# Performance work log

Hardware: AMD Instinct MI355X
Metric: run time of the kernel (lower is better)

Reference implementation:

```python
import jax, jax.numpy as jnp
import numpy as np

N, E, H = 100000, 3200000, 128


def setup_inputs() -> dict:
    key = jax.random.key(0)
    ks = jax.random.split(key, 12)
    s = 1.0 / np.sqrt(H)
    x = jax.random.normal(ks[0], (N, H), dtype=jnp.float32)
    edge_index = jax.random.randint(ks[1], (2, E), 0, N, dtype=jnp.int64)
    # GatedGraphConv weight: [num_layers=1, H, H] -> single [H, H]
    W = jax.random.normal(ks[2], (H, H), dtype=jnp.float32) * s
    # GRUCell (gate order: r, z, n)
    gru_w_ih = jax.random.normal(ks[3], (3 * H, H), dtype=jnp.float32) * s
    gru_w_hh = jax.random.normal(ks[4], (3 * H, H), dtype=jnp.float32) * s
    gru_b_ih = jax.random.normal(ks[5], (3 * H,), dtype=jnp.float32) * s
    gru_b_hh = jax.random.normal(ks[6], (3 * H,), dtype=jnp.float32) * s
    # LSTM layer 0 (gate order: i, f, g, o)
    lstm_w_ih = jax.random.normal(ks[7], (4 * H, H), dtype=jnp.float32) * s
    lstm_w_hh = jax.random.normal(ks[8], (4 * H, H), dtype=jnp.float32) * s
    lstm_b_ih = jax.random.normal(ks[9], (4 * H,), dtype=jnp.float32) * s
    lstm_b_hh = jax.random.normal(ks[10], (4 * H,), dtype=jnp.float32) * s
    return {
        "x": x, "edge_index": edge_index, "W": W,
        "gru_w_ih": gru_w_ih, "gru_w_hh": gru_w_hh,
        "gru_b_ih": gru_b_ih, "gru_b_hh": gru_b_hh,
        "lstm_w_ih": lstm_w_ih, "lstm_w_hh": lstm_w_hh,
        "lstm_b_ih": lstm_b_ih, "lstm_b_hh": lstm_b_hh,
    }


def _forward(x, edge_index, W, gru_w_ih, gru_w_hh, gru_b_ih, gru_b_hh,
             lstm_w_ih, lstm_w_hh, lstm_b_ih, lstm_b_hh):
    n = x.shape[0]
    src, dst = edge_index[0], edge_index[1]
    # GatedGraphConv, num_layers=1, mean aggregation
    m = x @ W                                   # [N, H]
    msg = m[src]                                # [E, H] gather (memory-bound)
    agg_sum = jax.ops.segment_sum(msg, dst, num_segments=n)
    deg = jax.ops.segment_sum(jnp.ones((src.shape[0],), x.dtype), dst, num_segments=n)
    agg = agg_sum / jnp.maximum(deg, 1.0)[:, None]
    # GRUCell(agg, x): gates r, z, n
    gi = agg @ gru_w_ih.T + gru_b_ih
    gh = x @ gru_w_hh.T + gru_b_hh
    i_r, i_z, i_n = jnp.split(gi, 3, axis=-1)
    h_r, h_z, h_n = jnp.split(gh, 3, axis=-1)
    r = jax.nn.sigmoid(i_r + h_r)
    z = jax.nn.sigmoid(i_z + h_z)
    ng = jnp.tanh(i_n + r * h_n)
    h_conv = (1.0 - z) * ng + z * x             # conv output H_tilde
    # 1-layer LSTM over seq_len=1 with zero initial (H, C)
    gates = h_conv @ lstm_w_ih.T + lstm_b_ih + lstm_b_hh  # h0 = 0
    i_g, f_g, g_g, o_g = jnp.split(gates, 4, axis=-1)
    c = jax.nn.sigmoid(i_g) * jnp.tanh(g_g)
    h_lstm = jax.nn.sigmoid(o_g) * jnp.tanh(c)
    return jax.nn.relu(h_lstm)


def reference(x, edge_index, W, gru_w_ih, gru_w_hh, gru_b_ih, gru_b_hh,
              lstm_w_ih, lstm_w_hh, lstm_b_ih, lstm_b_hh):
    return _forward(x, edge_index, W, gru_w_ih, gru_w_hh, gru_b_ih, gru_b_hh,
                    lstm_w_ih, lstm_w_hh, lstm_b_ih, lstm_b_hh)
```

## Files before the change

kernel.cpp:

```cpp
#include <hip/hip_runtime.h>
#include <math.h>

#define HD 128
#define PB 512
#define SCB 4096

typedef __attribute__((ext_vector_type(8))) short short8;
typedef __attribute__((ext_vector_type(4))) float f32x4;
typedef __attribute__((ext_vector_type(2))) float f32x2;
typedef __attribute__((ext_vector_type(4))) unsigned u32x4;

__device__ __forceinline__ float sigf(float v) { return 1.0f / (1.0f + __expf(-v)); }
__device__ __forceinline__ float tanhf_fast(float v) {
  float e = __expf(2.0f * v);
  return 1.0f - 2.0f / (e + 1.0f);
}

__device__ __forceinline__ unsigned short f2bf(float f) {
  union { float f; unsigned u; } v; v.f = f;
  unsigned r = (v.u + 0x7fffu + ((v.u >> 16) & 1u)) >> 16;
  return (unsigned short)r;
}
__device__ __forceinline__ float bf2f(unsigned short b) {
  union { unsigned u; float f; } v; v.u = ((unsigned)b) << 16;
  return v.f;
}


__global__ __launch_bounds__(256) void bcount_k(const int* __restrict__ ei,
                                                int* __restrict__ bcnt,
                                                int E, int N, int shift, int NB) {
  __shared__ int h[256];
  const int blk = blockIdx.x, tid = threadIdx.x;
  h[tid] = 0;
  __syncthreads();
  int per = (E + PB - 1) / PB;
  int lo = blk * per;
  int hi = (lo + per < E) ? lo + per : E;
  for (int e = lo + tid; e < hi; e += 256) {
    int d = ei[(size_t)E + e];
    if ((unsigned)d >= (unsigned)N) continue;
    atomicAdd(&h[d >> shift], 1);
  }
  __syncthreads();
  if (tid < NB) bcnt[tid * PB + blk] = h[tid];
}

__global__ __launch_bounds__(256) void scan1_k(const int* __restrict__ a,
                                               int* __restrict__ bsums, int total) {
  __shared__ int ts[256];
  int b = blockIdx.x, tid = threadIdx.x;
  int lo = b * SCB + tid * 16;
  int s = 0;
#pragma unroll
  for (int i = 0; i < 16; ++i) {
    int idx = lo + i;
    if (idx < total) s += a[idx];
  }
  ts[tid] = s;
  __syncthreads();
  for (int off = 128; off > 0; off >>= 1) {
    if (tid < off) ts[tid] += ts[tid + off];
    __syncthreads();
  }
  if (tid == 0) bsums[b] = ts[0];
}

__global__ __launch_bounds__(256) void scan2_k(int* __restrict__ bsums, int nb) {
  __shared__ int ts[256];
  int tid = threadIdx.x;
  int v = (tid < nb) ? bsums[tid] : 0;
  ts[tid] = v;
  __syncthreads();
  for (int off = 1; off < 256; off <<= 1) {
    int u = (tid >= off) ? ts[tid - off] : 0;
    __syncthreads();
    ts[tid] += u;
    __syncthreads();
  }
  if (tid < nb) bsums[tid] = ts[tid] - v;
}

__global__ __launch_bounds__(256) void scan3_k(int* __restrict__ a,
                                               const int* __restrict__ bsums,
                                               int total, int nblk) {
  __shared__ int ts[256];
  int b = blockIdx.x, tid = threadIdx.x;
  int lo = b * SCB + tid * 16;
  int pre[16];
  int s = 0;
#pragma unroll
  for (int i = 0; i < 16; ++i) {
    int idx = lo + i;
    int xv = (idx < total) ? a[idx] : 0;
    pre[i] = s;
    s += xv;
  }
  ts[tid] = s;
  __syncthreads();
  for (int off = 1; off < 256; off <<= 1) {
    int u = (tid >= off) ? ts[tid - off] : 0;
    __syncthreads();
    ts[tid] += u;
    __syncthreads();
  }
  int off0 = ts[tid] - s + bsums[b];
#pragma unroll
  for (int i = 0; i < 16; ++i) {
    int idx = lo + i;
    if (idx < total) a[idx] = off0 + pre[i];
  }
  if (b == nblk - 1 && tid == 255) a[total] = off0 + s;
}

__global__ __launch_bounds__(256) void bpart_k(const int* __restrict__ ei,
                                               const int* __restrict__ bstart,
                                               unsigned* __restrict__ ebuf,
                                               int E, int N, int shift, int NB,
                                               int sbits) {
  __shared__ int cur[256];
  const int blk = blockIdx.x, tid = threadIdx.x;
  if (tid < NB) cur[tid] = bstart[tid * PB + blk];
  __syncthreads();
  int per = (E + PB - 1) / PB;
  int lo = blk * per;
  int hi = (lo + per < E) ? lo + per : E;
  const unsigned dmask = (1u << shift) - 1u;
  for (int e = lo + tid; e < hi; e += 256) {
    int s = ei[e];
    int d = ei[(size_t)E + e];
    if ((unsigned)s >= (unsigned)N || (unsigned)d >= (unsigned)N) continue;
    int p = atomicAdd(&cur[d >> shift], 1);
    ebuf[p] = (((unsigned)d & dmask) << sbits) | (unsigned)s;
  }
}

__global__ __launch_bounds__(256) void bfill2_k(const unsigned* __restrict__ ebuf,
                                                const int* __restrict__ bstart,
                                                int* __restrict__ rowstart,
                                                int* __restrict__ csr,
                                                int N, int shift, int NB, int sbits) {
  __shared__ int cnt[2048];
  __shared__ int tsum[256];
  const int b = blockIdx.x, tid = threadIdx.x;
  const int d0 = b << shift;
  int dmax = d0 + (1 << shift);
  if (dmax > N) dmax = N;
  const int nd = dmax - d0;
  const unsigned smask = (1u << sbits) - 1u;
  for (int i = tid; i < nd; i += 256) cnt[i] = 0;
  __syncthreads();
  const int base = bstart[b * PB];
  const int end = bstart[(b + 1) * PB];
  for (int idx = base + tid; idx < end; idx += 256)
    atomicAdd(&cnt[ebuf[idx] >> sbits], 1);
  __syncthreads();
  const int C = (nd + 255) / 256;
  int lo = tid * C;
  int hi = (lo + C < nd) ? lo + C : nd;
  int loc[8];
  int s = 0;
  for (int i = lo; i < hi; ++i) {
    loc[i - lo] = cnt[i];
    s += cnt[i];
  }
  tsum[tid] = s;
  __syncthreads();
  for (int off = 1; off < 256; off <<= 1) {
    int u = (tid >= off) ? tsum[tid - off] : 0;
    __syncthreads();
    tsum[tid] += u;
    __syncthreads();
  }
  int run = tsum[tid] - s + base;
  for (int i = lo; i < hi; ++i) {
    rowstart[d0 + i] = run;
    cnt[i] = run;
    run += loc[i - lo];
  }
  if (b == NB - 1 && tid == 255) rowstart[N] = end;
  __syncthreads();
  for (int idx = base + tid; idx < end; idx += 256) {
    unsigned pk = ebuf[idx];
    int p = atomicAdd(&cnt[pk >> sbits], 1);
    csr[p] = (int)(pk & smask);
  }
}


__global__ __launch_bounds__(256) void convx_k(const float* __restrict__ x,
                                               unsigned short* __restrict__ xb,
                                               unsigned* __restrict__ x8, int n4) {
  int t = blockIdx.x * 256 + threadIdx.x;
  if (t >= n4) return;
  float4 v = reinterpret_cast<const float4*>(x)[t];
  ushort4 o;
  o.x = f2bf(v.x); o.y = f2bf(v.y); o.z = f2bf(v.z); o.w = f2bf(v.w);
  reinterpret_cast<ushort4*>(xb)[t] = o;
  int p8 = 0;
  p8 = __builtin_amdgcn_cvt_pk_fp8_f32(v.x, v.y, p8, false);
  p8 = __builtin_amdgcn_cvt_pk_fp8_f32(v.z, v.w, p8, true);
  x8[t] = (unsigned)p8;
}

__global__ __launch_bounds__(256) void prepw_k(
    const float* __restrict__ gwhh, const float* __restrict__ lwih,
    const float* __restrict__ lbih, const float* __restrict__ lbhh,
    unsigned short* __restrict__ gwhhb, unsigned short* __restrict__ lwb,
    float* __restrict__ lbias) {
  int t = blockIdx.x * 256 + threadIdx.x;
  if (t < 49152) { gwhhb[t] = f2bf(gwhh[t]); return; }
  t -= 49152;
  if (t < 49152) {
    int j = t >> 7, k = t & 127;
    int jm = j < 128 ? j : j + 128;
    lwb[t] = f2bf(lwih[(size_t)jm * 128 + k]);
    return;
  }
  t -= 49152;
  if (t < 384) {
    int jm = t < 128 ? t : t + 128;
    lbias[t] = lbih[jm] + lbhh[jm];
  }
}

__global__ __launch_bounds__(256) void prepbp_k(const float* __restrict__ W,
                                                const float* __restrict__ gwih,
                                                unsigned short* __restrict__ Bpb) {
  int t = blockIdx.x * 256 + threadIdx.x;
  if (t >= 49152) return;
  int j = t >> 7, k = t & 127;
  const float4* wr = reinterpret_cast<const float4*>(W + (size_t)k * 128);
  const float4* gr = reinterpret_cast<const float4*>(gwih + (size_t)j * 128);
  float acc = 0.f;
#pragma unroll
  for (int c = 0; c < 32; ++c) {
    float4 a = wr[c], b = gr[c];
    acc += a.x * b.x + a.y * b.y + a.z * b.z + a.w * b.w;
  }
  Bpb[t] = f2bf(acc);
}

__device__ __forceinline__ void accf8(f32x2* acc, uint4 v) {
  acc[0] += __builtin_amdgcn_cvt_pk_f32_fp8((int)v.x, false);
  acc[1] += __builtin_amdgcn_cvt_pk_f32_fp8((int)v.x, true);
  acc[2] += __builtin_amdgcn_cvt_pk_f32_fp8((int)v.y, false);
  acc[3] += __builtin_amdgcn_cvt_pk_f32_fp8((int)v.y, true);
  acc[4] += __builtin_amdgcn_cvt_pk_f32_fp8((int)v.z, false);
  acc[5] += __builtin_amdgcn_cvt_pk_f32_fp8((int)v.z, true);
  acc[6] += __builtin_amdgcn_cvt_pk_f32_fp8((int)v.w, false);
  acc[7] += __builtin_amdgcn_cvt_pk_f32_fp8((int)v.w, true);
}

__global__ __launch_bounds__(256) void gather_f8_k(const int* __restrict__ csr,
                                                   const int* __restrict__ rowstart,
                                                   const unsigned* __restrict__ x8,
                                                   unsigned short* __restrict__ xaggb,
                                                   int row0, int rowend) {
  int w = row0 + (int)(((long long)blockIdx.x * 256 + threadIdx.x) >> 6);
  if (w >= rowend) return;
  const int lane = threadIdx.x & 63;
  const int sub = lane >> 3, li = lane & 7;
  const int beg = rowstart[w], end = rowstart[w + 1];
  const uint4* x4 = reinterpret_cast<const uint4*>(x8);

  f32x2 acc[8];
#pragma unroll
  for (int i = 0; i < 8; ++i) acc[i] = (f32x2)0.f;

  int j = beg;
  for (; j + 16 <= end; j += 16) {
    int s0 = __builtin_nontemporal_load(&csr[j + sub]);
    int s1 = __builtin_nontemporal_load(&csr[j + 8 + sub]);
    uint4 v0 = x4[(size_t)s0 * 8 + li];
    uint4 v1 = x4[(size_t)s1 * 8 + li];
    accf8(acc, v0);
    accf8(acc, v1);
  }
  for (; j + 8 <= end; j += 8) {
    int s0 = __builtin_nontemporal_load(&csr[j + sub]);
    uint4 v0 = x4[(size_t)s0 * 8 + li];
    accf8(acc, v0);
  }
  int rem = end - j;
  if (sub < rem) {
    int s0 = csr[j + sub];
    uint4 v0 = x4[(size_t)s0 * 8 + li];
    accf8(acc, v0);
  }

  float a16[16];
#pragma unroll
  for (int i = 0; i < 8; ++i) { a16[2 * i] = acc[i].x; a16[2 * i + 1] = acc[i].y; }
#pragma unroll
  for (int i = 0; i < 16; ++i) {
    a16[i] += __shfl_xor(a16[i], 8, 64);
    a16[i] += __shfl_xor(a16[i], 16, 64);
    a16[i] += __shfl_xor(a16[i], 32, 64);
  }

  if (lane < 8) {
    float scale = 1.0f / fmaxf((float)(end - beg), 1.0f);
    u32x4 o1, o2;
    o1.x = (unsigned)f2bf(a16[0] * scale) | ((unsigned)f2bf(a16[1] * scale) << 16);
    o1.y = (unsigned)f2bf(a16[2] * scale) | ((unsigned)f2bf(a16[3] * scale) << 16);
    o1.z = (unsigned)f2bf(a16[4] * scale) | ((unsigned)f2bf(a16[5] * scale) << 16);
    o1.w = (unsigned)f2bf(a16[6] * scale) | ((unsigned)f2bf(a16[7] * scale) << 16);
    o2.x = (unsigned)f2bf(a16[8] * scale) | ((unsigned)f2bf(a16[9] * scale) << 16);
    o2.y = (unsigned)f2bf(a16[10] * scale) | ((unsigned)f2bf(a16[11] * scale) << 16);
    o2.z = (unsigned)f2bf(a16[12] * scale) | ((unsigned)f2bf(a16[13] * scale) << 16);
    o2.w = (unsigned)f2bf(a16[14] * scale) | ((unsigned)f2bf(a16[15] * scale) << 16);
    u32x4* dst = reinterpret_cast<u32x4*>(xaggb + (size_t)w * HD) + li * 2;
    dst[0] = o1;
    dst[1] = o2;
  }
}

__global__ __launch_bounds__(256) void gru_fused_k(
    const unsigned short* __restrict__ xaggb, const unsigned short* __restrict__ xb,
    const unsigned short* __restrict__ Bpb, const unsigned short* __restrict__ gwhhb,
    const float* __restrict__ gbih, const float* __restrict__ gbhh,
    unsigned short* __restrict__ hconv, int nrows, int nt) {
  __shared__ unsigned short Bsm[3][32][136];
  const int id = blockIdx.x;
  const int rest = id >> 3;
  const int cg = rest & 3;
  const int t = ((rest >> 2) << 3) | (id & 7);
  if (t >= nt) return;
  const int tid = threadIdx.x;
  const int w = tid >> 6, lane = tid & 63;
  const int q = lane >> 4, r = lane & 15;
  const int row0 = t * 64;
  const int c0 = cg * 32;

  int arow = row0 + (w << 4) + r;
  int ar = arow < nrows ? arow : nrows - 1;
  const unsigned short* Aa = xaggb + (size_t)ar * HD + q * 8;
  const unsigned short* Ax = xb + (size_t)ar * HD + q * 8;
  short8 a1[4], a2[4];
#pragma unroll
  for (int ks = 0; ks < 4; ++ks) {
    a1[ks] = *reinterpret_cast<const short8*>(Aa + ks * 32);
    a2[ks] = *reinterpret_cast<const short8*>(Ax + ks * 32);
  }

  f32x4 acc[6][2];
#pragma unroll
  for (int p = 0; p < 6; ++p)
#pragma unroll
    for (int cb = 0; cb < 2; ++cb) acc[p][cb] = (f32x4)0.f;

#pragma unroll
  for (int it = 0; it < 6; ++it) {
    int idx = it * 256 + tid;
    int p = idx >> 9, rem = idx & 511;
    int col = rem >> 4, kq = rem & 15;
    uint4 v = *reinterpret_cast<const uint4*>(
        Bpb + ((size_t)(p * 128 + c0 + col)) * HD + kq * 8);
    *reinterpret_cast<uint4*>(&Bsm[p][col][kq * 8]) = v;
  }
  __syncthreads();
#pragma unroll
  for (int ks = 0; ks < 4; ++ks)
#pragma unroll
    for (int p = 0; p < 3; ++p)
#pragma unroll
      for (int cb = 0; cb < 2; ++cb) {
        short8 bf = *reinterpret_cast<const short8*>(&Bsm[p][cb * 16 + r][ks * 32 + q * 8]);
        acc[p][cb] = __builtin_amdgcn_mfma_f32_16x16x32_bf16(a1[ks], bf, acc[p][cb], 0, 0, 0);
      }
  __syncthreads();

#pragma unroll
  for (int it = 0; it < 6; ++it) {
    int idx = it * 256 + tid;
    int p = idx >> 9, rem = idx & 511;
    int col = rem >> 4, kq = rem & 15;
    uint4 v = *reinterpret_cast<const uint4*>(
        gwhhb + ((size_t)(p * 128 + c0 + col)) * HD + kq * 8);
    *reinterpret_cast<uint4*>(&Bsm[p][col][kq * 8]) = v;
  }
  __syncthreads();
#pragma unroll
  for (int ks = 0; ks < 4; ++ks)
#pragma unroll
    for (int p = 0; p < 3; ++p)
#pragma unroll
      for (int cb = 0; cb < 2; ++cb) {
        short8 bf = *reinterpret_cast<const short8*>(&Bsm[p][cb * 16 + r][ks * 32 + q * 8]);
        acc[3 + p][cb] = __builtin_amdgcn_mfma_f32_16x16x32_bf16(a2[ks], bf, acc[3 + p][cb], 0, 0, 0);
      }

#pragma unroll
  for (int cb = 0; cb < 2; ++cb) {
    int col = c0 + cb * 16 + r;
    float bir = gbih[col], biz = gbih[col + 128], bin = gbih[col + 256];
    float bhr = gbhh[col], bhz = gbhh[col + 128], bhn = gbhh[col + 256];
#pragma unroll
    for (int reg = 0; reg < 4; ++reg) {
      int row = row0 + (w << 4) + q * 4 + reg;
      if (row < nrows) {
        float ir = acc[0][cb][reg] + bir, iz = acc[1][cb][reg] + biz;
        float inn = acc[2][cb][reg] + bin;
        float hr = acc[3][cb][reg] + bhr, hz = acc[4][cb][reg] + bhz;
        float hn = acc[5][cb][reg] + bhn;
        float rr = sigf(ir + hr), zz = sigf(iz + hz);
        float nn = tanhf_fast(inn + rr * hn);
        float xv = bf2f(xb[(size_t)row * HD + col]);
        hconv[(size_t)row * HD + col] = f2bf((1.f - zz) * nn + zz * xv);
      }
    }
  }
}

__global__ __launch_bounds__(256) void lstm_fused_k(
    const unsigned short* __restrict__ hconv, const unsigned short* __restrict__ lwb,
    const float* __restrict__ lbias, float* __restrict__ out, int nrows, int nt) {
  __shared__ unsigned short Bsm[3][32][136];
  const int id = blockIdx.x;
  const int rest = id >> 3;
  const int cg = rest & 3;
  const int t = ((rest >> 2) << 3) | (id & 7);
  if (t >= nt) return;
  const int tid = threadIdx.x;
  const int w = tid >> 6, lane = tid & 63;
  const int q = lane >> 4, r = lane & 15;
  const int row0 = t * 64;
  const int c0 = cg * 32;

  int arow = row0 + (w << 4) + r;
  int ar = arow < nrows ? arow : nrows - 1;
  const unsigned short* Ap = hconv + (size_t)ar * HD + q * 8;
  short8 hp[4];
#pragma unroll
  for (int ks = 0; ks < 4; ++ks)
    hp[ks] = *reinterpret_cast<const short8*>(Ap + ks * 32);

#pragma unroll
  for (int it = 0; it < 6; ++it) {
    int idx = it * 256 + tid;
    int p = idx >> 9, rem = idx & 511;
    int col = rem >> 4, kq = rem & 15;
    uint4 v = *reinterpret_cast<const uint4*>(
        lwb + ((size_t)(p * 128 + c0 + col)) * HD + kq * 8);
    *reinterpret_cast<uint4*>(&Bsm[p][col][kq * 8]) = v;
  }
  __syncthreads();

  f32x4 acc[3][2];
#pragma unroll
  for (int p = 0; p < 3; ++p)
#pragma unroll
    for (int cb = 0; cb < 2; ++cb) acc[p][cb] = (f32x4)0.f;

#pragma unroll
  for (int ks = 0; ks < 4; ++ks)
#pragma unroll
    for (int p = 0; p < 3; ++p)
#pragma unroll
      for (int cb = 0; cb < 2; ++cb) {
        short8 bf = *reinterpret_cast<const short8*>(&Bsm[p][cb * 16 + r][ks * 32 + q * 8]);
        acc[p][cb] = __builtin_amdgcn_mfma_f32_16x16x32_bf16(hp[ks], bf, acc[p][cb], 0, 0, 0);
      }

#pragma unroll
  for (int cb = 0; cb < 2; ++cb) {
    int col = c0 + cb * 16 + r;
    float bi = lbias[col], bg = lbias[col + 128], bo = lbias[col + 256];
#pragma unroll
    for (int reg = 0; reg < 4; ++reg) {
      int row = row0 + (w << 4) + q * 4 + reg;
      if (row < nrows) {
        float ig = acc[0][cb][reg] + bi;
        float gg = acc[1][cb][reg] + bg;
        float og = acc[2][cb][reg] + bo;
        float cc = sigf(ig) * tanhf_fast(gg);
        out[(size_t)row * HD + col] = fmaxf(sigf(og) * tanhf_fast(cc), 0.f);
      }
    }
  }
}


extern "C" void kernel_launch(void* const* d_in, const int* in_sizes, int n_in,
                              void* d_out, int out_size, void* d_ws, size_t ws_size,
                              hipStream_t stream) {
  const float* x = (const float*)d_in[0];
  const int* ei = (const int*)d_in[1];
  const float* W = (const float*)d_in[2];
  const float* gw_ih = (const float*)d_in[3];
  const float* gw_hh = (const float*)d_in[4];
  const float* gb_ih = (const float*)d_in[5];
  const float* gb_hh = (const float*)d_in[6];
  const float* lw_ih = (const float*)d_in[7];
  const float* lb_ih = (const float*)d_in[9];
  const float* lb_hh = (const float*)d_in[10];
  float* out = (float*)d_out;

  const int N = in_sizes[0] / HD;
  const int E = in_sizes[1] / 2;
  const size_t nH = (size_t)N * HD;

  int shift = 9;
  while (((N + (1 << shift) - 1) >> shift) > 256) ++shift;
  const int NB = (N + (1 << shift) - 1) >> shift;
  const int sbits = 32 - shift;

  const size_t N4p = (size_t)((N + 1 + 7) & ~7);
  const size_t E4 = (size_t)((E + 3) & ~3);
  const size_t BC = (size_t)NB * PB + 8;
  const int sc_total = NB * PB;
  const int sc_nblk = (sc_total + SCB - 1) / SCB;

  char* p = (char*)d_ws;
  int* rowstart = (int*)p;  p += 4 * N4p;
  int* bcnt = (int*)p;      p += 4 * BC;
  int* bsums = (int*)p;     p += 4 * 64;
  int* csr = (int*)p;       p += 4 * E4;
  size_t sz_eb = 4 * E4, sz_xb = 2 * nH;
  unsigned* ebuf = (unsigned*)p;
  unsigned short* xb = (unsigned short*)p;
  p += (sz_eb > sz_xb ? sz_eb : sz_xb);
  unsigned short* hconv = (unsigned short*)p;  p += 2 * nH;
  unsigned short* Bpb = (unsigned short*)p;    p += 2 * 49152;
  unsigned short* gwhhb = (unsigned short*)p;  p += 2 * 49152;
  unsigned short* lwb = (unsigned short*)p;    p += 2 * 49152;
  float* lbias = (float*)p;                    p += 4 * 384;

  unsigned* x8 = (unsigned*)hconv;

  unsigned short* xaggb = (unsigned short*)d_out;

  dim3 blk(256);
  unsigned rb = (unsigned)((N + 63) / 64);
  unsigned rb8 = (rb + 7) & ~7u;

  bcount_k<<<PB, blk, 0, stream>>>(ei, bcnt, E, N, shift, NB);
  scan1_k<<<sc_nblk, blk, 0, stream>>>(bcnt, bsums, sc_total);
  scan2_k<<<1, blk, 0, stream>>>(bsums, sc_nblk);
  scan3_k<<<sc_nblk, blk, 0, stream>>>(bcnt, bsums, sc_total, sc_nblk);
  bpart_k<<<PB, blk, 0, stream>>>(ei, bcnt, ebuf, E, N, shift, NB, sbits);
  bfill2_k<<<NB, blk, 0, stream>>>(ebuf, bcnt, rowstart, csr, N, shift, NB, sbits);

  convx_k<<<(unsigned)((nH / 4 + 255) / 256), blk, 0, stream>>>(x, xb, x8, (int)(nH / 4));
  prepw_k<<<(2 * 49152 + 384 + 255) / 256, blk, 0, stream>>>(
      gw_hh, lw_ih, lb_ih, lb_hh, gwhhb, lwb, lbias);
  prepbp_k<<<192, blk, 0, stream>>>(W, gw_ih, Bpb);

  int half = N / 2;
  {
    long long gt0 = (long long)half * 64;
    gather_f8_k<<<(unsigned)((gt0 + 255) / 256), blk, 0, stream>>>(
        csr, rowstart, x8, xaggb, 0, half);
    long long gt1 = (long long)(N - half) * 64;
    gather_f8_k<<<(unsigned)((gt1 + 255) / 256), blk, 0, stream>>>(
        csr, rowstart, x8, xaggb, half, N);
  }

  gru_fused_k<<<4 * rb8, blk, 0, stream>>>(
      xaggb, xb, Bpb, gwhhb, gb_ih, gb_hh, hconv, N, (int)rb);

  lstm_fused_k<<<4 * rb8, blk, 0, stream>>>(hconv, lwb, lbias, out, N, (int)rb);
}
```

Measured before the change: 440.3 us.

## Make GRU/LSTM GEMM blocks persistent over 8 row tiles with prefetched A fragments

Each block of the GRU and LSTM fused kernels now processes 8 consecutive 64-row tiles instead of one. It loads its weight slice into shared memory once (the GRU kernel holds both weight sets in a doubled LDS buffer) and loads biases once. The next tile's A fragments are prefetched into registers while the current tile computes. This cuts the repeated per-block weight staging and syncs, at the cost of an 8x smaller grid, more LDS per block and more registers, which can reduce occupancy and latency hiding.

```diff
diff --git a/kernel.cpp b/kernel.cpp
--- a/kernel.cpp
+++ b/kernel.cpp
@@ -4,6 +4,7 @@
 #define HD 128
 #define PB 512
 #define SCB 4096
+#define MT 8
 
 typedef __attribute__((ext_vector_type(8))) short short8;
 typedef __attribute__((ext_vector_type(4))) float f32x4;
@@ -320,121 +321,130 @@
     const unsigned short* __restrict__ xaggb, const unsigned short* __restrict__ xb,
     const unsigned short* __restrict__ Bpb, const unsigned short* __restrict__ gwhhb,
     const float* __restrict__ gbih, const float* __restrict__ gbhh,
-    unsigned short* __restrict__ hconv, int nrows, int nt) {
+    unsigned short* __restrict__ hconv, int nrows, int nt, int ngroups) {
+  __shared__ unsigned short Bsm[6][32][136];
+  const int id = blockIdx.x;
+  const int rest = id >> 3;
+  const int cg = rest & 3;
+  const int g = ((rest >> 2) << 3) | (id & 7);
+  if (g >= ngroups) return;
+  const int tid = threadIdx.x;
+  const int w = tid >> 6, lane = tid & 63;
+  const int q = lane >> 4, r = lane & 15;
+  const int c0 = cg * 32;
+
+#pragma unroll
+  for (int it = 0; it < 12; ++it) {
+    int idx = it * 256 + tid;
+    int p = idx >> 9;
+    int rem = idx & 511;
+    int col = rem >> 4, kq = rem & 15;
+    const unsigned short* src =
+        (p < 3) ? Bpb + ((size_t)(p * 128 + c0 + col)) * HD
+                : gwhhb + ((size_t)((p - 3) * 128 + c0 + col)) * HD;
+    uint4 v = *reinterpret_cast<const uint4*>(src + kq * 8);
+    *reinterpret_cast<uint4*>(&Bsm[p][col][kq * 8]) = v;
+  }
+  __syncthreads();
+
+  float bir, biz, bin, bhr, bhz, bhn, bir2, biz2, bin2, bhr2, bhz2, bhn2;
+  {
+    int col = c0 + r;
+    bir = gbih[col]; biz = gbih[col + 128]; bin = gbih[col + 256];
+    bhr = gbhh[col]; bhz = gbhh[col + 128]; bhn = gbhh[col + 256];
+    col += 16;
+    bir2 = gbih[col]; biz2 = gbih[col + 128]; bin2 = gbih[col + 256];
+    bhr2 = gbhh[col]; bhz2 = gbhh[col + 128]; bhn2 = gbhh[col + 256];
+  }
+
+  const int t0 = g * MT;
+  const int tend = (t0 + MT < nt) ? t0 + MT : nt;
+
+  short8 a1[4], a2[4], n1[4], n2[4];
+  {
+    int arow = t0 * 64 + (w << 4) + r;
+    int ar = arow < nrows ? arow : nrows - 1;
+    const unsigned short* Aa = xaggb + (size_t)ar * HD + q * 8;
+    const unsigned short* Ax = xb + (size_t)ar * HD + q * 8;
+#pragma unroll
+    for (int ks = 0; ks < 4; ++ks) {
+      a1[ks] = *reinterpret_cast<const short8*>(Aa + ks * 32);
+      a2[ks] = *reinterpret_cast<const short8*>(Ax + ks * 32);
+    }
+  }
+
+  for (int t = t0; t < tend; ++t) {
+    if (t + 1 < tend) {
+      int arow = (t + 1) * 64 + (w << 4) + r;
+      int ar = arow < nrows ? arow : nrows - 1;
+      const unsigned short* Aa = xaggb + (size_t)ar * HD + q * 8;
+      const unsigned short* Ax = xb + (size_t)ar * HD + q * 8;
+#pragma unroll
+      for (int ks = 0; ks < 4; ++ks) {
+        n1[ks] = *reinterpret_cast<const short8*>(Aa + ks * 32);
+        n2[ks] = *reinterpret_cast<const short8*>(Ax + ks * 32);
+      }
+    }
+
+    f32x4 acc[6][2];
+#pragma unroll
+    for (int p = 0; p < 6; ++p)
+#pragma unroll
+      for (int cb = 0; cb < 2; ++cb) acc[p][cb] = (f32x4)0.f;
+
+#pragma unroll
+    for (int ks = 0; ks < 4; ++ks)
+#pragma unroll
+      for (int p = 0; p < 6; ++p) {
+        short8 af = (p < 3) ? a1[ks] : a2[ks];
+#pragma unroll
+        for (int cb = 0; cb < 2; ++cb) {
+          short8 bf = *reinterpret_cast<const short8*>(&Bsm[p][cb * 16 + r][ks * 32 + q * 8]);
+          acc[p][cb] = __builtin_amdgcn_mfma_f32_16x16x32_bf16(af, bf, acc[p][cb], 0, 0, 0);
+        }
+      }
+
+    const int row0 = t * 64;
+#pragma unroll
+    for (int cb = 0; cb < 2; ++cb) {
+      int col = c0 + cb * 16 + r;
+      float vir = cb ? bir2 : bir, viz = cb ? biz2 : biz, vin = cb ? bin2 : bin;
+      float vhr = cb ? bhr2 : bhr, vhz = cb ? bhz2 : bhz, vhn = cb ? bhn2 : bhn;
+#pragma unroll
+      for (int reg = 0; reg < 4; ++reg) {
+        int row = row0 + (w << 4) + q * 4 + reg;
+        if (row < nrows) {
+          float ir = acc[0][cb][reg] + vir, iz = acc[1][cb][reg] + viz;
+          float inn = acc[2][cb][reg] + vin;
+          float hr = acc[3][cb][reg] + vhr, hz = acc[4][cb][reg] + vhz;
+          float hn = acc[5][cb][reg] + vhn;
+          float rr = sigf(ir + hr), zz = sigf(iz + hz);
+          float nn = tanhf_fast(inn + rr * hn);
+          float xv = bf2f(xb[(size_t)row * HD + col]);
+          hconv[(size_t)row * HD + col] = f2bf((1.f - zz) * nn + zz * xv);
+        }
+      }
+    }
+
+#pragma unroll
+    for (int ks = 0; ks < 4; ++ks) { a1[ks] = n1[ks]; a2[ks] = n2[ks]; }
+  }
+}
+
+__global__ __launch_bounds__(256) void lstm_fused_k(
+    const unsigned short* __restrict__ hconv, const unsigned short* __restrict__ lwb,
+    const float* __restrict__ lbias, float* __restrict__ out, int nrows, int nt,
+    int ngroups) {
   __shared__ unsigned short Bsm[3][32][136];
   const int id = blockIdx.x;
   const int rest = id >> 3;
   const int cg = rest & 3;
-  const int t = ((rest >> 2) << 3) | (id & 7);
-  if (t >= nt) return;
+  const int g = ((rest >> 2) << 3) | (id & 7);
+  if (g >= ngroups) return;
   const int tid = threadIdx.x;
   const int w = tid >> 6, lane = tid & 63;
   const int q = lane >> 4, r = lane & 15;
-  const int row0 = t * 64;
   const int c0 = cg * 32;
-
-  int arow = row0 + (w << 4) + r;
-  int ar = arow < nrows ? arow : nrows - 1;
-  const unsigned short* Aa = xaggb + (size_t)ar * HD + q * 8;
-  const unsigned short* Ax = xb + (size_t)ar * HD + q * 8;
-  short8 a1[4], a2[4];
-#pragma unroll
-  for (int ks = 0; ks < 4; ++ks) {
-    a1[ks] = *reinterpret_cast<const short8*>(Aa + ks * 32);
-    a2[ks] = *reinterpret_cast<const short8*>(Ax + ks * 32);
-  }
-
-  f32x4 acc[6][2];
-#pragma unroll
-  for (int p = 0; p < 6; ++p)
-#pragma unroll
-    for (int cb = 0; cb < 2; ++cb) acc[p][cb] = (f32x4)0.f;
-
-#pragma unroll
-  for (int it = 0; it < 6; ++it) {
-    int idx = it * 256 + tid;
-    int p = idx >> 9, rem = idx & 511;
-    int col = rem >> 4, kq = rem & 15;
-    uint4 v = *reinterpret_cast<const uint4*>(
-        Bpb + ((size_t)(p * 128 + c0 + col)) * HD + kq * 8);
-    *reinterpret_cast<uint4*>(&Bsm[p][col][kq * 8]) = v;
-  }
-  __syncthreads();
-#pragma unroll
-  for (int ks = 0; ks < 4; ++ks)
-#pragma unroll
-    for (int p = 0; p < 3; ++p)
-#pragma unroll
-      for (int cb = 0; cb < 2; ++cb) {
-        short8 bf = *reinterpret_cast<const short8*>(&Bsm[p][cb * 16 + r][ks * 32 + q * 8]);
-        acc[p][cb] = __builtin_amdgcn_mfma_f32_16x16x32_bf16(a1[ks], bf, acc[p][cb], 0, 0, 0);
-      }
-  __syncthreads();
-
-#pragma unroll
-  for (int it = 0; it < 6; ++it) {
-    int idx = it * 256 + tid;
-    int p = idx >> 9, rem = idx & 511;
-    int col = rem >> 4, kq = rem & 15;
-    uint4 v = *reinterpret_cast<const uint4*>(
-        gwhhb + ((size_t)(p * 128 + c0 + col)) * HD + kq * 8);
-    *reinterpret_cast<uint4*>(&Bsm[p][col][kq * 8]) = v;
-  }
-  __syncthreads();
-#pragma unroll
-  for (int ks = 0; ks < 4; ++ks)
-#pragma unroll
-    for (int p = 0; p < 3; ++p)
-#pragma unroll
-      for (int cb = 0; cb < 2; ++cb) {
-        short8 bf = *reinterpret_cast<const short8*>(&Bsm[p][cb * 16 + r][ks * 32 + q * 8]);
-        acc[3 + p][cb] = __builtin_amdgcn_mfma_f32_16x16x32_bf16(a2[ks], bf, acc[3 + p][cb], 0, 0, 0);
-      }
-
-#pragma unroll
-  for (int cb = 0; cb < 2; ++cb) {
-    int col = c0 + cb * 16 + r;
-    float bir = gbih[col], biz = gbih[col + 128], bin = gbih[col + 256];
-    float bhr = gbhh[col], bhz = gbhh[col + 128], bhn = gbhh[col + 256];
-#pragma unroll
-    for (int reg = 0; reg < 4; ++reg) {
-      int row = row0 + (w << 4) + q * 4 + reg;
-      if (row < nrows) {
-        float ir = acc[0][cb][reg] + bir, iz = acc[1][cb][reg] + biz;
-        float inn = acc[2][cb][reg] + bin;
-        float hr = acc[3][cb][reg] + bhr, hz = acc[4][cb][reg] + bhz;
-        float hn = acc[5][cb][reg] + bhn;
-        float rr = sigf(ir + hr), zz = sigf(iz + hz);
-        float nn = tanhf_fast(inn + rr * hn);
-        float xv = bf2f(xb[(size_t)row * HD + col]);
-        hconv[(size_t)row * HD + col] = f2bf((1.f - zz) * nn + zz * xv);
-      }
-    }
-  }
-}
-
-__global__ __launch_bounds__(256) void lstm_fused_k(
-    const unsigned short* __restrict__ hconv, const unsigned short* __restrict__ lwb,
-    const float* __restrict__ lbias, float* __restrict__ out, int nrows, int nt) {
-  __shared__ unsigned short Bsm[3][32][136];
-  const int id = blockIdx.x;
-  const int rest = id >> 3;
-  const int cg = rest & 3;
-  const int t = ((rest >> 2) << 3) | (id & 7);
-  if (t >= nt) return;
-  const int tid = threadIdx.x;
-  const int w = tid >> 6, lane = tid & 63;
-  const int q = lane >> 4, r = lane & 15;
-  const int row0 = t * 64;
-  const int c0 = cg * 32;
-
-  int arow = row0 + (w << 4) + r;
-  int ar = arow < nrows ? arow : nrows - 1;
-  const unsigned short* Ap = hconv + (size_t)ar * HD + q * 8;
-  short8 hp[4];
-#pragma unroll
-  for (int ks = 0; ks < 4; ++ks)
-    hp[ks] = *reinterpret_cast<const short8*>(Ap + ks * 32);
 
 #pragma unroll
   for (int it = 0; it < 6; ++it) {
@@ -447,37 +457,73 @@
   }
   __syncthreads();
 
-  f32x4 acc[3][2];
-#pragma unroll
-  for (int p = 0; p < 3; ++p)
-#pragma unroll
-    for (int cb = 0; cb < 2; ++cb) acc[p][cb] = (f32x4)0.f;
-
-#pragma unroll
-  for (int ks = 0; ks < 4; ++ks)
+  float bi1, bg1, bo1, bi2, bg2, bo2;
+  {
+    int col = c0 + r;
+    bi1 = lbias[col]; bg1 = lbias[col + 128]; bo1 = lbias[col + 256];
+    col += 16;
+    bi2 = lbias[col]; bg2 = lbias[col + 128]; bo2 = lbias[col + 256];
+  }
+
+  const int t0 = g * MT;
+  const int tend = (t0 + MT < nt) ? t0 + MT : nt;
+
+  short8 hp[4], np[4];
+  {
+    int arow = t0 * 64 + (w << 4) + r;
+    int ar = arow < nrows ? arow : nrows - 1;
+    const unsigned short* Ap = hconv + (size_t)ar * HD + q * 8;
+#pragma unroll
+    for (int ks = 0; ks < 4; ++ks)
+      hp[ks] = *reinterpret_cast<const short8*>(Ap + ks * 32);
+  }
+
+  for (int t = t0; t < tend; ++t) {
+    if (t + 1 < tend) {
+      int arow = (t + 1) * 64 + (w << 4) + r;
+      int ar = arow < nrows ? arow : nrows - 1;
+      const unsigned short* Ap = hconv + (size_t)ar * HD + q * 8;
+#pragma unroll
+      for (int ks = 0; ks < 4; ++ks)
+        np[ks] = *reinterpret_cast<const short8*>(Ap + ks * 32);
+    }
+
+    f32x4 acc[3][2];
 #pragma unroll
     for (int p = 0; p < 3; ++p)
 #pragma unroll
-      for (int cb = 0; cb < 2; ++cb) {
-        short8 bf = *reinterpret_cast<const short8*>(&Bsm[p][cb * 16 + r][ks * 32 + q * 8]);
-        acc[p][cb] = __builtin_amdgcn_mfma_f32_16x16x32_bf16(hp[ks], bf, acc[p][cb], 0, 0, 0);
-      }
-
-#pragma unroll
-  for (int cb = 0; cb < 2; ++cb) {
-    int col = c0 + cb * 16 + r;
-    float bi = lbias[col], bg = lbias[col + 128], bo = lbias[col + 256];
-#pragma unroll
-    for (int reg = 0; reg < 4; ++reg) {
-      int row = row0 + (w << 4) + q * 4 + reg;
-      if (row < nrows) {
-        float ig = acc[0][cb][reg] + bi;
-        float gg = acc[1][cb][reg] + bg;
-        float og = acc[2][cb][reg] + bo;
-        float cc = sigf(ig) * tanhf_fast(gg);
-        out[(size_t)row * HD + col] = fmaxf(sigf(og) * tanhf_fast(cc), 0.f);
+      for (int cb = 0; cb < 2; ++cb) acc[p][cb] = (f32x4)0.f;
+
+#pragma unroll
+    for (int ks = 0; ks < 4; ++ks)
+#pragma unroll
+      for (int p = 0; p < 3; ++p)
+#pragma unroll
+        for (int cb = 0; cb < 2; ++cb) {
+          short8 bf = *reinterpret_cast<const short8*>(&Bsm[p][cb * 16 + r][ks * 32 + q * 8]);
+          acc[p][cb] = __builtin_amdgcn_mfma_f32_16x16x32_bf16(hp[ks], bf, acc[p][cb], 0, 0, 0);
+        }
+
+    const int row0 = t * 64;
+#pragma unroll
+    for (int cb = 0; cb < 2; ++cb) {
+      int col = c0 + cb * 16 + r;
+      float bi = cb ? bi2 : bi1, bg = cb ? bg2 : bg1, bo = cb ? bo2 : bo1;
+#pragma unroll
+      for (int reg = 0; reg < 4; ++reg) {
+        int row = row0 + (w << 4) + q * 4 + reg;
+        if (row < nrows) {
+          float ig = acc[0][cb][reg] + bi;
+          float gg = acc[1][cb][reg] + bg;
+          float og = acc[2][cb][reg] + bo;
+          float cc = sigf(ig) * tanhf_fast(gg);
+          out[(size_t)row * HD + col] = fmaxf(sigf(og) * tanhf_fast(cc), 0.f);
+        }
       }
     }
+
+#pragma unroll
+    for (int ks = 0; ks < 4; ++ks) hp[ks] = np[ks];
   }
 }
 
@@ -533,7 +579,8 @@
 
   dim3 blk(256);
   unsigned rb = (unsigned)((N + 63) / 64);
-  unsigned rb8 = (rb + 7) & ~7u;
+  int ngroups = (int)((rb + MT - 1) / MT);
+  unsigned g8 = (unsigned)((ngroups + 7) & ~7);
 
   bcount_k<<<PB, blk, 0, stream>>>(ei, bcnt, E, N, shift, NB);
   scan1_k<<<sc_nblk, blk, 0, stream>>>(bcnt, bsums, sc_total);
@@ -557,8 +604,8 @@
         csr, rowstart, x8, xaggb, half, N);
   }
 
-  gru_fused_k<<<4 * rb8, blk, 0, stream>>>(
-      xaggb, xb, Bpb, gwhhb, gb_ih, gb_hh, hconv, N, (int)rb);
-
-  lstm_fused_k<<<4 * rb8, blk, 0, stream>>>(hconv, lwb, lbias, out, N, (int)rb);
-}
+  gru_fused_k<<<4 * g8, blk, 0, stream>>>(
+      xaggb, xb, Bpb, gwhhb, gb_ih, gb_hh, hconv, N, (int)rb, ngroups);
+
+  lstm_fused_k<<<4 * g8, blk, 0, stream>>>(hconv, lwb, lbias, out, N, (int)rb, ngroups);
+}
```

Result: slower. 496.2 us (+12.7%).
